# Kernel optimization log

Hardware: AMD Instinct MI355X
Metric: run time of the kernel (lower is better)

## Reference

```python
import jax, jax.numpy as jnp
import numpy as np

B, S, L, D, H = 8, 512, 15, 768, 512
PRUNE_RATIO = 0.2
K = int(PRUNE_RATIO * S)  # fixed max number of pruned spans (102)


def setup_inputs() -> dict:
    key = jax.random.key(0)
    ks = jax.random.split(key, 8)
    span_vecs = jax.random.normal(ks[0], (B, S, L, D), dtype=jnp.float32)
    sequence_lengths = jax.random.randint(ks[1], (B,), S // 2, S + 1)
    span_begin = jnp.broadcast_to(jnp.arange(S)[None, :, None], (B, S, L)).astype(jnp.int32)
    span_end = span_begin + jnp.arange(L, dtype=jnp.int32)[None, None, :]
    # valid span: end position inside the sequence
    span_mask = (span_end < sequence_lengths[:, None, None]).astype(jnp.float32)
    sc = 0.02
    w1 = jax.random.normal(ks[2], (D, H), jnp.float32) * sc
    b1 = jnp.zeros((H,), jnp.float32)
    w2 = jax.random.normal(ks[3], (H, H), jnp.float32) * sc
    b2 = jnp.zeros((H,), jnp.float32)
    w3 = jax.random.normal(ks[4], (H, 1), jnp.float32) * sc
    b3 = jnp.zeros((1,), jnp.float32)
    return dict(span_vecs=span_vecs, span_mask=span_mask, span_begin=span_begin,
                span_end=span_end, sequence_lengths=sequence_lengths,
                w1=w1, b1=b1, w2=w2, b2=b2, w3=w3, b3=b3)


def reference(span_vecs, span_mask, span_begin, span_end, sequence_lengths,
              w1, b1, w2, b2, w3, b3):
    # 3-layer MLP scorer (dropout p=0 -> identity)
    h = jax.nn.relu(jnp.einsum('bsld,dh->bslh', span_vecs, w1) + b1)
    h = jax.nn.relu(jnp.einsum('bslh,hk->bslk', h, w2) + b2)
    prune_scores = jnp.einsum('bslh,ho->bslo', h, w3) + b3            # [B,S,L,1]
    prune_scores = prune_scores - (1.0 - span_mask[..., None]) * 10000.0

    # prune_spans: per-batch top-k over flattened [S*L] span grid
    flat = prune_scores.reshape(B, S * L)
    _, idx = jax.lax.top_k(flat, K)                                   # [B,K]
    idx = jnp.sort(idx, axis=-1)                                      # sort_after_pruning
    span_lengths = jnp.minimum(
        (PRUNE_RATIO * sequence_lengths.astype(jnp.float32)).astype(jnp.int32), K)

    # filter_spans: gather along the flattened span axis
    def gather(x):
        return jnp.take_along_axis(x.reshape(B, S * L, -1), idx[..., None], axis=1)

    f_vecs = gather(span_vecs)                                        # [B,K,D]
    f_scores = gather(prune_scores)                                   # [B,K,1]
    f_begin = gather(span_begin)                                      # [B,K,1]
    f_end = gather(span_end)                                          # [B,K,1]

    # create_masks: validity per pruned slot + square / lower-triangular masks
    valid = (jnp.arange(K)[None, :] < span_lengths[:, None])          # [B,K]
    square_mask = (valid[:, :, None] & valid[:, None, :]).astype(jnp.float32)
    triangular_mask = square_mask * jnp.tril(jnp.ones((K, K), jnp.float32))[None]
    return (prune_scores, idx, f_vecs, f_scores, f_begin, f_end,
            span_lengths, square_mask, triangular_mask)
```

## Files before the change

kernel.cpp:

```cpp
#include <hip/hip_runtime.h>
#include <cstddef>
#include <cstdint>

#define B_    8
#define S_    512
#define L_    15
#define D_    768
#define H_    512
#define KTOP  102
#define SL_   (S_ * L_)
#define M_    (B_ * SL_)

#define OFF_SCORES 0
#define OFF_IDX    61440
#define OFF_FVECS  62256
#define OFF_FSC    688944
#define OFF_FBEG   689760
#define OFF_FEND   690576
#define OFF_SLEN   691392
#define OFF_SQ     691400
#define OFF_TRI    774632

typedef _Float16 f16;
typedef __attribute__((ext_vector_type(4))) _Float16 f16x4;
typedef __attribute__((ext_vector_type(8))) _Float16 f16x8;
typedef __attribute__((ext_vector_type(16))) float f32x16;

__device__ f16   g_W1h[512 * 768], g_W1l[512 * 768];
__device__ f16   g_W2h[512 * 512], g_W2l[512 * 512];
__device__ f16   g_h1h[(size_t)M_ * H_];
__device__ f16   g_h1l[(size_t)M_ * H_];
__device__ float g_scores[M_];

__device__ __forceinline__ int swz(int L) { return L ^ (((L >> 9) & 3) << 4); }

__device__ __forceinline__ void gl_lds16(const void* gsrc, void* ldst) {
  __builtin_amdgcn_global_load_lds(
      (const __attribute__((address_space(1))) void*)gsrc,
      (__attribute__((address_space(3))) void*)ldst, 16, 0, 0);
}

__device__ __forceinline__ f16 hi16(float x) { return (f16)x; }
__device__ __forceinline__ f16 lo16(float x) { return (f16)(x - (float)((f16)x)); }

__global__ void prep_kernel(const float* __restrict__ W1, const float* __restrict__ W2) {
  int e = blockIdx.x * 256 + threadIdx.x;
  if (e < 768 * 512) {
    int k = e >> 9, n = e & 511;
    float x = W1[e];
    g_W1h[n * 768 + k] = hi16(x);
    g_W1l[n * 768 + k] = lo16(x);
  } else {
    e -= 768 * 512;
    if (e < 512 * 512) {
      int k = e >> 9, n = e & 511;
      float x = W2[e];
      g_W2h[n * 512 + k] = hi16(x);
      g_W2l[n * 512 + k] = lo16(x);
    }
  }
}

__global__ void init_kernel() {
  g_scores[blockIdx.x * 256 + threadIdx.x] = 0.0f;
}

template <int LAYER>
__global__ __launch_bounds__(256, 2)
void gemm_kernel(const float* __restrict__ V,
                 const float* __restrict__ bias,
                 const float* __restrict__ w3) {
  constexpr int K = (LAYER == 1) ? 768 : 512;
  __shared__ __align__(16) char lds[32 * 1024];
  char* Ah = lds;
  char* Al = lds + 8192;
  char* Bh = lds + 16384;
  char* Bl = lds + 24576;

  const int t = threadIdx.x;
  const int lane = t & 63;
  const int w = t >> 6;
  const int wm = w >> 1, wn = w & 1;

  const int o = (blockIdx.x & 7) * 240 + (blockIdx.x >> 3);
  const int nb = o & 3, mb = o >> 2;
  const int m0 = mb * 128, n0 = nb * 128;

  const f16* WH = (LAYER == 1) ? g_W1h : g_W2h;
  const f16* WL = (LAYER == 1) ? g_W1l : g_W2l;

  f32x16 acc[2][2];
  #pragma unroll
  for (int i = 0; i < 2; ++i)
    #pragma unroll
    for (int j = 0; j < 2; ++j) acc[i][j] = (f32x16)0.0f;

  for (int k0 = 0; k0 < K; k0 += 32) {
    #pragma unroll
    for (int h = 0; h < 2; ++h) {
      int P = (h * 4 + w) * 1024 + lane * 16;
      int Lg = swz(P);
      int r = Lg >> 6, q = (Lg >> 4) & 3;
      size_t go = (size_t)(n0 + r) * K + k0 + q * 8;
      gl_lds16(WH + go, Bh + P);
      gl_lds16(WL + go, Bl + P);
    }
    if (LAYER == 1) {
      int row = t >> 1;
      int ks = (t & 1) * 16;
      const float* src = V + (size_t)(m0 + row) * 768 + k0 + ks;
      float4 vv[4];
      vv[0] = *(const float4*)(src);
      vv[1] = *(const float4*)(src + 4);
      vv[2] = *(const float4*)(src + 8);
      vv[3] = *(const float4*)(src + 12);
      #pragma unroll
      for (int j = 0; j < 4; ++j) {
        f16x4 hv, lv;
        hv[0] = hi16(vv[j].x); lv[0] = lo16(vv[j].x);
        hv[1] = hi16(vv[j].y); lv[1] = lo16(vv[j].y);
        hv[2] = hi16(vv[j].z); lv[2] = lo16(vv[j].z);
        hv[3] = hi16(vv[j].w); lv[3] = lo16(vv[j].w);
        int P = swz(row * 64 + (ks + j * 4) * 2);
        *(f16x4*)(Ah + P) = hv;
        *(f16x4*)(Al + P) = lv;
      }
    } else {
      #pragma unroll
      for (int h = 0; h < 2; ++h) {
        int P = (h * 4 + w) * 1024 + lane * 16;
        int Lg = swz(P);
        int r = Lg >> 6, q = (Lg >> 4) & 3;
        size_t go = (size_t)(m0 + r) * 512 + k0 + q * 8;
        gl_lds16(g_h1h + go, Ah + P);
        gl_lds16(g_h1l + go, Al + P);
      }
    }
    __syncthreads();
    #pragma unroll
    for (int kk = 0; kk < 2; ++kk) {
      const int intra = kk * 32 + (lane >> 5) * 16;
      f16x8 ah[2], al[2], bh[2], bl[2];
      #pragma unroll
      for (int mt = 0; mt < 2; ++mt) {
        int P = swz((wm * 64 + mt * 32 + (lane & 31)) * 64 + intra);
        ah[mt] = *(const f16x8*)(Ah + P);
        al[mt] = *(const f16x8*)(Al + P);
      }
      #pragma unroll
      for (int nt = 0; nt < 2; ++nt) {
        int P = swz((wn * 64 + nt * 32 + (lane & 31)) * 64 + intra);
        bh[nt] = *(const f16x8*)(Bh + P);
        bl[nt] = *(const f16x8*)(Bl + P);
      }
      #pragma unroll
      for (int mt = 0; mt < 2; ++mt)
        #pragma unroll
        for (int nt = 0; nt < 2; ++nt) {
          acc[mt][nt] = __builtin_amdgcn_mfma_f32_32x32x16_f16(ah[mt], bh[nt], acc[mt][nt], 0, 0, 0);
          acc[mt][nt] = __builtin_amdgcn_mfma_f32_32x32x16_f16(al[mt], bh[nt], acc[mt][nt], 0, 0, 0);
          acc[mt][nt] = __builtin_amdgcn_mfma_f32_32x32x16_f16(ah[mt], bl[nt], acc[mt][nt], 0, 0, 0);
        }
    }
    __syncthreads();
  }

  const int half = lane >> 5;
  if (LAYER == 1) {
    #pragma unroll
    for (int mt = 0; mt < 2; ++mt)
      #pragma unroll
      for (int nt = 0; nt < 2; ++nt) {
        int col = n0 + wn * 64 + nt * 32 + (lane & 31);
        float bb = bias[col];
        #pragma unroll
        for (int r = 0; r < 16; ++r) {
          int m = m0 + wm * 64 + mt * 32 + (r & 3) + ((r >> 2) << 3) + (half << 2);
          float v = fmaxf(acc[mt][nt][r] + bb, 0.0f);
          g_h1h[(size_t)m * 512 + col] = hi16(v);
          g_h1l[(size_t)m * 512 + col] = lo16(v);
        }
      }
  } else {
    #pragma unroll
    for (int mt = 0; mt < 2; ++mt) {
      float s[16];
      #pragma unroll
      for (int r = 0; r < 16; ++r) s[r] = 0.0f;
      #pragma unroll
      for (int nt = 0; nt < 2; ++nt) {
        int col = n0 + wn * 64 + nt * 32 + (lane & 31);
        float bb = bias[col];
        float wv = w3[col];
        #pragma unroll
        for (int r = 0; r < 16; ++r)
          s[r] += fmaxf(acc[mt][nt][r] + bb, 0.0f) * wv;
      }
      #pragma unroll
      for (int off = 1; off < 32; off <<= 1)
        #pragma unroll
        for (int r = 0; r < 16; ++r) s[r] += __shfl_xor(s[r], off, 64);
      if ((lane & 31) == 0) {
        #pragma unroll
        for (int r = 0; r < 16; ++r) {
          int m = m0 + wm * 64 + mt * 32 + (r & 3) + ((r >> 2) << 3) + (half << 2);
          atomicAdd(&g_scores[m], s[r]);
        }
      }
    }
  }
}

__global__ void finalize_kernel(const float* __restrict__ mask, const float* __restrict__ B3,
                                float* __restrict__ out) {
  int i = blockIdx.x * 256 + threadIdx.x;
  out[OFF_SCORES + i] = g_scores[i] + B3[0] - (1.0f - mask[i]) * 10000.0f;
}

__global__ void topk_kernel(const float* __restrict__ scores,
                            const int* __restrict__ seqlen,
                            float* __restrict__ out,
                            int* __restrict__ ws_idx,
                            int* __restrict__ ws_sl) {
  __shared__ float vals[SL_];
  __shared__ float rv[4];
  __shared__ int ri[4];
  __shared__ int sel[KTOP];

  const int t = threadIdx.x;
  const int b = blockIdx.x;
  const float* s = scores + (size_t)b * SL_;

  for (int i = t; i < SL_; i += 256) vals[i] = s[i];
  __syncthreads();

  for (int it = 0; it < KTOP; ++it) {
    float bv = -3.0e38f;
    int bi = 0x7fffffff;
    for (int i = t; i < SL_; i += 256) {
      float v = vals[i];
      if (v > bv) { bv = v; bi = i; }
    }
    #pragma unroll
    for (int off = 32; off > 0; off >>= 1) {
      float ov = __shfl_down(bv, off, 64);
      int oi = __shfl_down(bi, off, 64);
      if (ov > bv || (ov == bv && oi < bi)) { bv = ov; bi = oi; }
    }
    if ((t & 63) == 0) { rv[t >> 6] = bv; ri[t >> 6] = bi; }
    __syncthreads();
    if (t == 0) {
      float fb = rv[0]; int fi = ri[0];
      #pragma unroll
      for (int wv = 1; wv < 4; ++wv)
        if (rv[wv] > fb || (rv[wv] == fb && ri[wv] < fi)) { fb = rv[wv]; fi = ri[wv]; }
      sel[it] = fi;
      vals[fi] = -3.0e38f;
    }
    __syncthreads();
  }

  for (int pass = 0; pass < KTOP; ++pass) {
    int i = 2 * t + (pass & 1);
    if (i + 1 < KTOP) {
      int a = sel[i], c = sel[i + 1];
      if (a > c) { sel[i] = c; sel[i + 1] = a; }
    }
    __syncthreads();
  }

  if (t < KTOP) {
    out[OFF_IDX + b * KTOP + t] = (float)sel[t];
    ws_idx[b * KTOP + t] = sel[t];
  }
  if (t == 0) {
    int len = seqlen[b];
    int v = (int)(0.2f * (float)len);
    if (v > KTOP) v = KTOP;
    out[OFF_SLEN + b] = (float)v;
    ws_sl[b] = v;
  }
}

__global__ void gather_kernel(const float* __restrict__ V,
                              const int* __restrict__ sbeg,
                              const int* __restrict__ send,
                              float* __restrict__ out,
                              const int* __restrict__ ws_idx) {
  const int blk = blockIdx.x;
  const int b = blk / KTOP;
  const int t = threadIdx.x;
  const int sid = ws_idx[blk];
  const float4* s4 = reinterpret_cast<const float4*>(V + ((size_t)b * SL_ + sid) * D_);
  float4* d4 = reinterpret_cast<float4*>(out + OFF_FVECS + (size_t)blk * D_);
  d4[t] = s4[t];
  if (t == 0) {
    int gi = b * SL_ + sid;
    out[OFF_FSC + blk] = out[OFF_SCORES + gi];
    out[OFF_FBEG + blk] = (float)sbeg[gi];
    out[OFF_FEND + blk] = (float)send[gi];
  }
}

__global__ void masks_kernel(float* __restrict__ out, const int* __restrict__ ws_sl) {
  int e = blockIdx.x * 256 + threadIdx.x;
  if (e >= B_ * KTOP * KTOP) return;
  int b = e / (KTOP * KTOP);
  int r = e - b * (KTOP * KTOP);
  int i = r / KTOP;
  int j = r - i * KTOP;
  int len = ws_sl[b];
  float sq = (i < len && j < len) ? 1.0f : 0.0f;
  out[OFF_SQ + e] = sq;
  out[OFF_TRI + e] = (j <= i) ? sq : 0.0f;
}

extern "C" void kernel_launch(void* const* d_in, const int* in_sizes, int n_in,
                              void* d_out, int out_size, void* d_ws, size_t ws_size,
                              hipStream_t stream) {
  const float* V    = (const float*)d_in[0];
  const float* mask = (const float*)d_in[1];
  const int*   sbeg = (const int*)d_in[2];
  const int*   send = (const int*)d_in[3];
  const int*   slen = (const int*)d_in[4];
  const float* W1 = (const float*)d_in[5];
  const float* B1 = (const float*)d_in[6];
  const float* W2 = (const float*)d_in[7];
  const float* B2 = (const float*)d_in[8];
  const float* W3 = (const float*)d_in[9];
  const float* B3 = (const float*)d_in[10];
  float* out = (float*)d_out;
  int* ws_idx = (int*)d_ws;
  int* ws_sl = ws_idx + B_ * KTOP;

  prep_kernel<<<2560, 256, 0, stream>>>(W1, W2);
  init_kernel<<<240, 256, 0, stream>>>();
  gemm_kernel<1><<<1920, 256, 0, stream>>>(V, B1, nullptr);
  gemm_kernel<2><<<1920, 256, 0, stream>>>(nullptr, B2, W3);
  finalize_kernel<<<240, 256, 0, stream>>>(mask, B3, out);
  topk_kernel<<<B_, 256, 0, stream>>>(out, slen, out, ws_idx, ws_sl);
  gather_kernel<<<B_ * KTOP, 192, 0, stream>>>(V, sbeg, send, out, ws_idx);
  masks_kernel<<<(B_ * KTOP * KTOP + 255) / 256, 256, 0, stream>>>(out, ws_sl);
}
```

Before: 716.4 us.

## Double-buffer GEMM LDS tiles, tile weight transpose, replace score atomics with partials

The GEMM main loop now double-buffers its LDS tiles in a 64KB buffer. The next k-slice's async loads (and, for layer 1, register loads of V) are issued before computing on the current slice, which drops one barrier per iteration and overlaps memory with MFMA. Weight prep becomes an LDS-tiled transpose so global writes are coalesced. The LDS swizzle pattern changes. Score reduction writes 8 per-column-block partial arrays that finalize sums, instead of using atomics plus an init kernel. Doubling LDS to 64KB may limit occupancy to 2 blocks per CU, which the launch bounds already target.

After: 735.0 us. +2.6%, slower.

```diff
diff --git a/kernel.cpp b/kernel.cpp
--- a/kernel.cpp
+++ b/kernel.cpp
@@ -30,9 +30,9 @@
 __device__ f16   g_W2h[512 * 512], g_W2l[512 * 512];
 __device__ f16   g_h1h[(size_t)M_ * H_];
 __device__ f16   g_h1l[(size_t)M_ * H_];
-__device__ float g_scores[M_];
-
-__device__ __forceinline__ int swz(int L) { return L ^ (((L >> 9) & 3) << 4); }
+__device__ float g_part[8][M_];
+
+__device__ __forceinline__ int swz(int L) { return L ^ (((L >> 7) & 3) << 4); }
 
 __device__ __forceinline__ void gl_lds16(const void* gsrc, void* ldst) {
   __builtin_amdgcn_global_load_lds(
@@ -44,38 +44,37 @@
 __device__ __forceinline__ f16 lo16(float x) { return (f16)(x - (float)((f16)x)); }
 
 __global__ void prep_kernel(const float* __restrict__ W1, const float* __restrict__ W2) {
-  int e = blockIdx.x * 256 + threadIdx.x;
-  if (e < 768 * 512) {
-    int k = e >> 9, n = e & 511;
-    float x = W1[e];
-    g_W1h[n * 768 + k] = hi16(x);
-    g_W1l[n * 768 + k] = lo16(x);
-  } else {
-    e -= 768 * 512;
-    if (e < 512 * 512) {
-      int k = e >> 9, n = e & 511;
-      float x = W2[e];
-      g_W2h[n * 512 + k] = hi16(x);
-      g_W2l[n * 512 + k] = lo16(x);
-    }
-  }
-}
-
-__global__ void init_kernel() {
-  g_scores[blockIdx.x * 256 + threadIdx.x] = 0.0f;
+  __shared__ float LS[64][65];
+  int bid = blockIdx.x;
+  const float* W; f16 *GH, *GL; int K;
+  int tk, tn;
+  if (bid < 96) { W = W1; GH = g_W1h; GL = g_W1l; K = 768; tk = bid >> 3; tn = bid & 7; }
+  else { bid -= 96; W = W2; GH = g_W2h; GL = g_W2l; K = 512; tk = bid >> 3; tn = bid & 7; }
+  const int k0 = tk * 64, n0 = tn * 64;
+  const int t = threadIdx.x;
+  #pragma unroll
+  for (int s = 0; s < 16; ++s) {
+    int r = s * 4 + (t >> 6);
+    LS[r][t & 63] = W[(size_t)(k0 + r) * 512 + n0 + (t & 63)];
+  }
+  __syncthreads();
+  #pragma unroll
+  for (int s = 0; s < 16; ++s) {
+    int n = s * 4 + (t >> 6);
+    int k = t & 63;
+    float x = LS[k][n];
+    GH[(size_t)(n0 + n) * K + k0 + k] = hi16(x);
+    GL[(size_t)(n0 + n) * K + k0 + k] = lo16(x);
+  }
 }
 
 template <int LAYER>
 __global__ __launch_bounds__(256, 2)
-void gemm_kernel(const float* __restrict__ V,
-                 const float* __restrict__ bias,
+void gemm_kernel(const float* __restrict__ V, const float* __restrict__ bias,
                  const float* __restrict__ w3) {
   constexpr int K = (LAYER == 1) ? 768 : 512;
-  __shared__ __align__(16) char lds[32 * 1024];
-  char* Ah = lds;
-  char* Al = lds + 8192;
-  char* Bh = lds + 16384;
-  char* Bl = lds + 24576;
+  constexpr int NT = K / 32;
+  __shared__ __align__(16) char lds[65536];
 
   const int t = threadIdx.x;
   const int lane = t & 63;
@@ -95,7 +94,9 @@
     #pragma unroll
     for (int j = 0; j < 2; ++j) acc[i][j] = (f32x16)0.0f;
 
-  for (int k0 = 0; k0 < K; k0 += 32) {
+  auto stageB = [&](int it) {
+    const int k0 = it * 32;
+    char* Bh = lds + (it & 1) * 32768 + 16384;
     #pragma unroll
     for (int h = 0; h < 2; ++h) {
       int P = (h * 4 + w) * 1024 + lane * 16;
@@ -103,40 +104,48 @@
       int r = Lg >> 6, q = (Lg >> 4) & 3;
       size_t go = (size_t)(n0 + r) * K + k0 + q * 8;
       gl_lds16(WH + go, Bh + P);
-      gl_lds16(WL + go, Bl + P);
-    }
-    if (LAYER == 1) {
-      int row = t >> 1;
-      int ks = (t & 1) * 16;
-      const float* src = V + (size_t)(m0 + row) * 768 + k0 + ks;
-      float4 vv[4];
-      vv[0] = *(const float4*)(src);
-      vv[1] = *(const float4*)(src + 4);
-      vv[2] = *(const float4*)(src + 8);
-      vv[3] = *(const float4*)(src + 12);
-      #pragma unroll
-      for (int j = 0; j < 4; ++j) {
-        f16x4 hv, lv;
-        hv[0] = hi16(vv[j].x); lv[0] = lo16(vv[j].x);
-        hv[1] = hi16(vv[j].y); lv[1] = lo16(vv[j].y);
-        hv[2] = hi16(vv[j].z); lv[2] = lo16(vv[j].z);
-        hv[3] = hi16(vv[j].w); lv[3] = lo16(vv[j].w);
-        int P = swz(row * 64 + (ks + j * 4) * 2);
-        *(f16x4*)(Ah + P) = hv;
-        *(f16x4*)(Al + P) = lv;
-      }
-    } else {
-      #pragma unroll
-      for (int h = 0; h < 2; ++h) {
-        int P = (h * 4 + w) * 1024 + lane * 16;
-        int Lg = swz(P);
-        int r = Lg >> 6, q = (Lg >> 4) & 3;
-        size_t go = (size_t)(m0 + r) * 512 + k0 + q * 8;
-        gl_lds16(g_h1h + go, Ah + P);
-        gl_lds16(g_h1l + go, Al + P);
-      }
-    }
-    __syncthreads();
+      gl_lds16(WL + go, Bh + 8192 + P);
+    }
+  };
+  auto stageA2 = [&](int it) {
+    const int k0 = it * 32;
+    char* Ah = lds + (it & 1) * 32768;
+    #pragma unroll
+    for (int h = 0; h < 2; ++h) {
+      int P = (h * 4 + w) * 1024 + lane * 16;
+      int Lg = swz(P);
+      int r = Lg >> 6, q = (Lg >> 4) & 3;
+      size_t go = (size_t)(m0 + r) * 512 + k0 + q * 8;
+      gl_lds16(g_h1h + go, Ah + P);
+      gl_lds16(g_h1l + go, Ah + 8192 + P);
+    }
+  };
+  auto loadA1 = [&](int it, float4* vv) {
+    const int k0 = it * 32;
+    const int row = t >> 1, ks = (t & 1) * 16;
+    const float* src = V + (size_t)(m0 + row) * 768 + k0 + ks;
+    vv[0] = *(const float4*)(src);
+    vv[1] = *(const float4*)(src + 4);
+    vv[2] = *(const float4*)(src + 8);
+    vv[3] = *(const float4*)(src + 12);
+  };
+  auto writeA1 = [&](int it, const float4* vv) {
+    char* Ah = lds + (it & 1) * 32768;
+    const int row = t >> 1, ks = (t & 1) * 16;
+    #pragma unroll
+    for (int j = 0; j < 4; ++j) {
+      f16x4 hv, lv;
+      hv[0] = hi16(vv[j].x); lv[0] = lo16(vv[j].x);
+      hv[1] = hi16(vv[j].y); lv[1] = lo16(vv[j].y);
+      hv[2] = hi16(vv[j].z); lv[2] = lo16(vv[j].z);
+      hv[3] = hi16(vv[j].w); lv[3] = lo16(vv[j].w);
+      int P = swz(row * 64 + (ks + j * 4) * 2);
+      *(f16x4*)(Ah + P) = hv;
+      *(f16x4*)(Ah + 8192 + P) = lv;
+    }
+  };
+  auto compute = [&](int it) {
+    const char* base = lds + (it & 1) * 32768;
     #pragma unroll
     for (int kk = 0; kk < 2; ++kk) {
       const int intra = kk * 32 + (lane >> 5) * 16;
@@ -144,14 +153,14 @@
       #pragma unroll
       for (int mt = 0; mt < 2; ++mt) {
         int P = swz((wm * 64 + mt * 32 + (lane & 31)) * 64 + intra);
-        ah[mt] = *(const f16x8*)(Ah + P);
-        al[mt] = *(const f16x8*)(Al + P);
+        ah[mt] = *(const f16x8*)(base + P);
+        al[mt] = *(const f16x8*)(base + 8192 + P);
       }
       #pragma unroll
       for (int nt = 0; nt < 2; ++nt) {
         int P = swz((wn * 64 + nt * 32 + (lane & 31)) * 64 + intra);
-        bh[nt] = *(const f16x8*)(Bh + P);
-        bl[nt] = *(const f16x8*)(Bl + P);
+        bh[nt] = *(const f16x8*)(base + 16384 + P);
+        bl[nt] = *(const f16x8*)(base + 24576 + P);
       }
       #pragma unroll
       for (int mt = 0; mt < 2; ++mt)
@@ -162,6 +171,21 @@
           acc[mt][nt] = __builtin_amdgcn_mfma_f32_32x32x16_f16(ah[mt], bl[nt], acc[mt][nt], 0, 0, 0);
         }
     }
+  };
+
+  float4 vv[4];
+  if (LAYER == 1) { loadA1(0, vv); stageB(0); writeA1(0, vv); }
+  else { stageB(0); stageA2(0); }
+  __syncthreads();
+
+  for (int it = 0; it < NT; ++it) {
+    const bool nx = (it + 1 < NT);
+    if (nx) {
+      stageB(it + 1);
+      if (LAYER == 1) loadA1(it + 1, vv); else stageA2(it + 1);
+    }
+    compute(it);
+    if (nx && LAYER == 1) writeA1(it + 1, vv);
     __syncthreads();
   }
 
@@ -204,7 +228,7 @@
         #pragma unroll
         for (int r = 0; r < 16; ++r) {
           int m = m0 + wm * 64 + mt * 32 + (r & 3) + ((r >> 2) << 3) + (half << 2);
-          atomicAdd(&g_scores[m], s[r]);
+          g_part[nb * 2 + wn][m] = s[r];
         }
       }
     }
@@ -214,7 +238,10 @@
 __global__ void finalize_kernel(const float* __restrict__ mask, const float* __restrict__ B3,
                                 float* __restrict__ out) {
   int i = blockIdx.x * 256 + threadIdx.x;
-  out[OFF_SCORES + i] = g_scores[i] + B3[0] - (1.0f - mask[i]) * 10000.0f;
+  float s = 0.0f;
+  #pragma unroll
+  for (int p = 0; p < 8; ++p) s += g_part[p][i];
+  out[OFF_SCORES + i] = s + B3[0] - (1.0f - mask[i]) * 10000.0f;
 }
 
 __global__ void topk_kernel(const float* __restrict__ scores,
@@ -333,8 +360,7 @@
   int* ws_idx = (int*)d_ws;
   int* ws_sl = ws_idx + B_ * KTOP;
 
-  prep_kernel<<<2560, 256, 0, stream>>>(W1, W2);
-  init_kernel<<<240, 256, 0, stream>>>();
+  prep_kernel<<<160, 256, 0, stream>>>(W1, W2);
   gemm_kernel<1><<<1920, 256, 0, stream>>>(V, B1, nullptr);
   gemm_kernel<2><<<1920, 256, 0, stream>>>(nullptr, B2, W3);
   finalize_kernel<<<240, 256, 0, stream>>>(mask, B3, out);
```
